# Optimization experiments

Measured on AMD Instinct MI355X. Metric: run time of the kernel, lower is better.

Reference implementation:

```python
import jax, jax.numpy as jnp
import numpy as np

H = 16
EPS = 1e-5

def _layernorm(x, gamma, beta):
    mu = jnp.mean(x, axis=-1, keepdims=True)
    var = jnp.var(x, axis=-1, keepdims=True)
    return (x - mu) * jax.lax.rsqrt(var + EPS) * gamma + beta

def setup_inputs() -> dict:
    key = jax.random.key(0)
    ks = jax.random.split(key, 5)
    B, T, E = 4, 2048, 1024
    D = E // H
    return {
        "x": jax.random.normal(ks[0], (B, T, E), dtype=jnp.float32),
        "Wqkv": jax.random.normal(ks[1], (E, 3 * E), dtype=jnp.float32) * (E ** -0.5),
        "bqkv": jax.random.normal(ks[2], (3 * E,), dtype=jnp.float32) * 0.02,
        "q_gamma": jnp.ones((D,), jnp.float32),
        "q_beta": jnp.zeros((D,), jnp.float32),
        "k_gamma": jnp.ones((D,), jnp.float32),
        "k_beta": jnp.zeros((D,), jnp.float32),
        "Wproj": jax.random.normal(ks[3], (E, E), dtype=jnp.float32) * (E ** -0.5),
        "bproj": jnp.zeros((E,), jnp.float32),
    }

def reference(x, Wqkv, bqkv, q_gamma, q_beta, k_gamma, k_beta, Wproj, bproj):
    B, T, E = x.shape
    D = E // H
    qkv = x @ Wqkv + bqkv                      # [B,T,3E]
    q, k, v = jnp.split(qkv, 3, axis=-1)
    # b t (h d) -> b h t d
    to_heads = lambda a: a.reshape(B, T, H, D).transpose(0, 2, 1, 3)
    q, k, v = to_heads(q), to_heads(k), to_heads(v)
    q = _layernorm(q, q_gamma, q_beta)
    k = _layernorm(k, k_gamma, k_beta)
    scale = 1.0 / jnp.sqrt(jnp.float32(D))
    scores = jnp.einsum('bhtd,bhsd->bhts', q, k) * scale   # [B,H,T,T]
    attn = jax.nn.softmax(scores, axis=-1)
    y = jnp.einsum('bhts,bhsd->bhtd', attn, v)             # [B,H,T,D]
    y = y.transpose(0, 2, 1, 3).reshape(B, T, E)           # b h t d -> b t (h d)
    return y @ Wproj + bproj
```

## Files before the change

### kernel.cpp

```cpp
#include <hip/hip_runtime.h>

#define Hn  16
#define Dh  64
#define Bb  4
#define Tn  2048
#define En  1024
#define Mn  8192
#define N1  3072
#define Kn  1024
#define BHT (Bb*Hn*Tn)

typedef __attribute__((ext_vector_type(8)))  short  short8;
typedef __attribute__((ext_vector_type(4)))  short  short4v;
typedef __attribute__((ext_vector_type(4)))  float  f32x4;
typedef __attribute__((ext_vector_type(8)))  __bf16 bf16x8;

__device__ __forceinline__ float b2f(short s) {
  unsigned u = ((unsigned)(unsigned short)s) << 16;
  return __builtin_bit_cast(float, u);
}
__device__ __forceinline__ short f2b(float f) {
  unsigned u = __builtin_bit_cast(unsigned, f);
  u += 0x7fffu + ((u >> 16) & 1u);
  return (short)(u >> 16);
}
__device__ __forceinline__ f32x4 mfma16(short8 a, short8 b, f32x4 c) {
  return __builtin_amdgcn_mfma_f32_16x16x32_bf16(
      __builtin_bit_cast(bf16x8, a), __builtin_bit_cast(bf16x8, b), c, 0, 0, 0);
}
__device__ __forceinline__ void gload16(const void* g, void* l) {
  __builtin_amdgcn_global_load_lds(
      (const __attribute__((address_space(1))) unsigned int*)g,
      (__attribute__((address_space(3))) unsigned int*)l, 16, 0, 0);
}

__global__ __launch_bounds__(256) void cvt_x_kernel(const float* __restrict__ x,
                                                    short* __restrict__ xb) {
  const size_t i = ((size_t)blockIdx.x * 256 + threadIdx.x) * 8;
  f32x4 a = *(const f32x4*)&x[i];
  f32x4 b = *(const f32x4*)&x[i + 4];
  short8 o;
  o[0]=f2b(a[0]); o[1]=f2b(a[1]); o[2]=f2b(a[2]); o[3]=f2b(a[3]);
  o[4]=f2b(b[0]); o[5]=f2b(b[1]); o[6]=f2b(b[2]); o[7]=f2b(b[3]);
  *(short8*)&xb[i] = o;
}

__global__ __launch_bounds__(256) void transpose_w_kernel(const float* __restrict__ in,
                                                          short* __restrict__ out,
                                                          int R, int C) {
  __shared__ float tile[32][33];
  const int tid = threadIdx.x;
  const int c0 = blockIdx.x * 32, r0 = blockIdx.y * 32;
  const int lr = tid >> 3, lc = (tid & 7) * 4;
  f32x4 v = *(const f32x4*)&in[(size_t)(r0 + lr) * C + c0 + lc];
  tile[lr][lc] = v[0]; tile[lr][lc+1] = v[1]; tile[lr][lc+2] = v[2]; tile[lr][lc+3] = v[3];
  __syncthreads();
  const int oc = tid >> 3, orr = (tid & 7) * 4;
  short4v ov;
  ov[0] = f2b(tile[orr][oc]);   ov[1] = f2b(tile[orr+1][oc]);
  ov[2] = f2b(tile[orr+2][oc]); ov[3] = f2b(tile[orr+3][oc]);
  *(short4v*)&out[(size_t)(c0 + oc) * R + r0 + orr] = ov;
}

template<int MODE>
__global__ __launch_bounds__(256) void gemm_kernel(
    const short* __restrict__ A, const short* __restrict__ Bt,
    const float* __restrict__ bias, float* __restrict__ Cf,
    short* __restrict__ qo, short* __restrict__ ko2, short* __restrict__ vo,
    int N, int NBX, int cpx) {
  __shared__ short As[4096];
  __shared__ short Bs[4096];
  const int lin = blockIdx.x;
  const int swz = (lin & 7) * cpx + (lin >> 3);
  const int bx = swz % NBX, by = swz / NBX;
  const int tid = threadIdx.x, lane = tid & 63, w = tid >> 6;
  const int rowBase = by * 128, colBase = bx * 128;
  f32x4 acc[4][4] = {};
  const int srow = tid >> 2, sk = (tid & 3) << 3;
  const short* Ag = A  + (size_t)(rowBase + srow) * Kn + sk;
  const short* Bg = Bt + (size_t)(colBase + srow) * Kn + sk;
  short* AsW = As + w * 512;
  short* BsW = Bs + w * 512;
  const int ar = (w >> 1) * 64, bc = (w & 1) * 64;
  const int lg8 = (lane >> 4) * 8, lr = lane & 15;

  for (int kt = 0; kt < Kn; kt += 32) {
    __syncthreads();
    gload16(Ag + kt,            AsW);
    gload16(Ag + kt + 64 * Kn,  AsW + 2048);
    gload16(Bg + kt,            BsW);
    gload16(Bg + kt + 64 * Kn,  BsW + 2048);
    __syncthreads();
    short8 af[4], bfr[4];
#pragma unroll
    for (int m = 0; m < 4; ++m) af[m]  = *(const short8*)&As[(ar + m*16 + lr)*32 + lg8];
#pragma unroll
    for (int n = 0; n < 4; ++n) bfr[n] = *(const short8*)&Bs[(bc + n*16 + lr)*32 + lg8];
#pragma unroll
    for (int m = 0; m < 4; ++m)
#pragma unroll
      for (int n = 0; n < 4; ++n)
        acc[m][n] = mfma16(af[m], bfr[n], acc[m][n]);
  }

  const int gr0 = rowBase + ar + (lane >> 4) * 4;
  const int gc0 = colBase + bc + lr;
#pragma unroll
  for (int m = 0; m < 4; ++m) {
#pragma unroll
    for (int n = 0; n < 4; ++n) {
      const int gc = gc0 + n * 16;
      const float bb = bias[gc];
#pragma unroll
      for (int r = 0; r < 4; ++r) {
        const int gr = gr0 + m * 16 + r;
        const float v = acc[m][n][r] + bb;
        if (MODE == 0) {
          Cf[(size_t)gr * N + gc] = v;
        } else {
          const int which = gc >> 10, e = gc & 1023;
          const int hh = e >> 6, d = e & 63;
          const int bidx = gr >> 11, t = gr & 2047;
          const size_t idx = ((size_t)(bidx * Hn + hh) * Tn + t) * Dh + d;
          short* dst = (which == 0) ? qo : (which == 1) ? ko2 : vo;
          dst[idx] = f2b(v);
        }
      }
    }
  }
}

__global__ __launch_bounds__(256) void ln_qk_kernel(short* __restrict__ qp, short* __restrict__ kp,
                                                    const float* __restrict__ qg, const float* __restrict__ qb,
                                                    const float* __restrict__ kg, const float* __restrict__ kb) {
  const int lane = threadIdx.x & 63;
  const int rp = blockIdx.x * 4 + (threadIdx.x >> 6);
  const size_t base = (size_t)rp * 64 + lane;
  float xq = b2f(qp[base]);
  float xk = b2f(kp[base]);
  float sq = xq, sk = xk;
#pragma unroll
  for (int off = 1; off < 64; off <<= 1) { sq += __shfl_xor(sq, off); sk += __shfl_xor(sk, off); }
  const float muq = sq * (1.f/64), muk = sk * (1.f/64);
  const float dq = xq - muq, dk = xk - muk;
  float vq = dq * dq, vk = dk * dk;
#pragma unroll
  for (int off = 1; off < 64; off <<= 1) { vq += __shfl_xor(vq, off); vk += __shfl_xor(vk, off); }
  const float rq = rsqrtf(vq * (1.f/64) + 1e-5f);
  const float rk = rsqrtf(vk * (1.f/64) + 1e-5f);
  const float yq = (dq * rq * qg[lane] + qb[lane]) * (0.125f * 1.44269504088896f);
  const float yk =  dk * rk * kg[lane] + kb[lane];
  qp[base] = f2b(yq);
  kp[base] = f2b(yk);
}

__global__ __launch_bounds__(256) void transpose_v_kernel(const short* __restrict__ vp,
                                                          short* __restrict__ vt) {
  __shared__ short tile[64][72];
  const int tid = threadIdx.x;
  const int bh = blockIdx.y, jt = blockIdx.x;
  const short* src = vp + ((size_t)bh * Tn + jt * 64) * Dh;
#pragma unroll
  for (int i = 0; i < 4; ++i) {
    const int idx = i * 1024 + tid * 4;
    short4v v = *(const short4v*)&src[idx];
    const int r = idx >> 6, c = idx & 63;
    tile[r][c] = v[0]; tile[r][c+1] = v[1]; tile[r][c+2] = v[2]; tile[r][c+3] = v[3];
  }
  __syncthreads();
  short* dst = vt + (size_t)bh * Dh * Tn + jt * 64;
#pragma unroll
  for (int i = 0; i < 4; ++i) {
    const int idx = i * 1024 + tid * 4;
    const int d = idx >> 6, t0 = idx & 63;
    short4v v;
    v[0] = tile[t0][d]; v[1] = tile[t0+1][d]; v[2] = tile[t0+2][d]; v[3] = tile[t0+3][d];
    *(short4v*)&dst[(size_t)d * Tn + t0] = v;
  }
}

__global__ __launch_bounds__(256) void flash_kernel(
    const short* __restrict__ qp, const short* __restrict__ kp,
    const short* __restrict__ vt, short* __restrict__ y) {
  __shared__ short Ks[2][4096];
  __shared__ short Vs[2][4096];
  __shared__ short Ps[8192];
  const int tid = threadIdx.x, lane = tid & 63, w = tid >> 6;
  const int lr = lane & 15, lg = lane >> 4;

  const int j0 = blockIdx.x;
  const int xcd = j0 & 7, kk0 = j0 >> 3;
  const int bh = 8 * xcd + (kk0 & 7), qt = kk0 >> 3;

  const int qrow0 = qt * 128 + w * 32;
  const short* qbase = qp + ((size_t)bh * Tn + qrow0) * Dh;

  short8 aq[2][2];
#pragma unroll
  for (int m = 0; m < 2; ++m)
#pragma unroll
    for (int kk = 0; kk < 2; ++kk)
      aq[m][kk] = *(const short8*)&qbase[(m*16 + lr)*64 + kk*32 + lg*8];

  f32x4 o[2][4] = {};
  float mrow[2][4], lpart[2][4];
#pragma unroll
  for (int m = 0; m < 2; ++m)
#pragma unroll
    for (int r = 0; r < 4; ++r) { mrow[m][r] = -3e38f; lpart[m][r] = 0.f; }

  const int srow = tid >> 3;
  const int sc = (tid & 7) * 8;
  short* Pw = Ps + w * 2048;
  const short* kb = kp + (size_t)bh * Tn * Dh;
  const short* vb = vt + (size_t)bh * Dh * Tn;

#define STAGE(jt, bsel)                                                   \
  {                                                                       \
    _Pragma("unroll")                                                     \
    for (int i = 0; i < 2; ++i) {                                         \
      const int row = i * 32 + srow;                                      \
      const int scs = sc ^ ((row & 7) << 3);                              \
      gload16(kb + (size_t)((jt) * 64 + row) * Dh + scs,                  \
              &Ks[bsel][w * 512 + i * 2048]);                             \
      gload16(vb + (size_t)row * Tn + (jt) * 64 + scs,                    \
              &Vs[bsel][w * 512 + i * 2048]);                             \
    }                                                                     \
  }

  STAGE(0, 0);
  __syncthreads();

  for (int j = 0; j < Tn / 64; ++j) {
    const int cur = j & 1;
    if (j + 1 < Tn / 64) STAGE(j + 1, cur ^ 1);

    short8 bk[4][2];
#pragma unroll
    for (int n = 0; n < 4; ++n)
#pragma unroll
      for (int kk = 0; kk < 2; ++kk) {
        const int row = n * 16 + lr;
        bk[n][kk] = *(const short8*)&Ks[cur][row*64 + ((kk*32 + lg*8) ^ ((row & 7) << 3))];
      }
    f32x4 s[2][4] = {};
    __builtin_amdgcn_s_setprio(1);
#pragma unroll
    for (int m = 0; m < 2; ++m)
#pragma unroll
      for (int n = 0; n < 4; ++n) {
        s[m][n] = mfma16(aq[m][0], bk[n][0], s[m][n]);
        s[m][n] = mfma16(aq[m][1], bk[n][1], s[m][n]);
      }
    __builtin_amdgcn_s_setprio(0);

    float pm[2][4];
#pragma unroll
    for (int m = 0; m < 2; ++m)
#pragma unroll
      for (int r = 0; r < 4; ++r)
        pm[m][r] = fmaxf(fmaxf(s[m][0][r], s[m][1][r]), fmaxf(s[m][2][r], s[m][3][r]));
    int ok = 1;
#pragma unroll
    for (int m = 0; m < 2; ++m)
#pragma unroll
      for (int r = 0; r < 4; ++r)
        ok &= (pm[m][r] <= mrow[m][r] + 11.0f) ? 1 : 0;
    if (!__all(ok)) {
      float tm[2][4];
#pragma unroll
      for (int m = 0; m < 2; ++m)
#pragma unroll
        for (int r = 0; r < 4; ++r) tm[m][r] = pm[m][r];
#pragma unroll
      for (int off = 1; off < 16; off <<= 1)
#pragma unroll
        for (int m = 0; m < 2; ++m)
#pragma unroll
          for (int r = 0; r < 4; ++r)
            tm[m][r] = fmaxf(tm[m][r], __shfl_xor(tm[m][r], off));
#pragma unroll
      for (int m = 0; m < 2; ++m)
#pragma unroll
        for (int r = 0; r < 4; ++r) {
          const float mn = fmaxf(mrow[m][r], tm[m][r]);
          const float corr = __builtin_amdgcn_exp2f(mrow[m][r] - mn);
          lpart[m][r] *= corr;
#pragma unroll
          for (int dn = 0; dn < 4; ++dn) o[m][dn][r] *= corr;
          mrow[m][r] = mn;
        }
    }

#pragma unroll
    for (int m = 0; m < 2; ++m)
#pragma unroll
      for (int n = 0; n < 4; ++n)
#pragma unroll
        for (int r = 0; r < 4; ++r) {
          const float p = __builtin_amdgcn_exp2f(s[m][n][r] - mrow[m][r]);
          const unsigned u = __builtin_bit_cast(unsigned, p);
          lpart[m][r] += __builtin_bit_cast(float, u & 0xffff0000u);
          const int q = m*16 + lg*4 + r;
          const int k = n*16 + lr;
          Pw[q*64 + (k ^ ((q & 7) << 3))] = (short)(u >> 16);
        }

    short8 pa[2][2], bv[4][2];
#pragma unroll
    for (int m = 0; m < 2; ++m)
#pragma unroll
      for (int kk = 0; kk < 2; ++kk) {
        const int q = m*16 + lr;
        pa[m][kk] = *(const short8*)&Pw[q*64 + ((kk*32 + lg*8) ^ ((q & 7) << 3))];
      }
#pragma unroll
    for (int dn = 0; dn < 4; ++dn)
#pragma unroll
      for (int kk = 0; kk < 2; ++kk) {
        const int row = dn * 16 + lr;
        bv[dn][kk] = *(const short8*)&Vs[cur][row*64 + ((kk*32 + lg*8) ^ ((row & 7) << 3))];
      }
    __builtin_amdgcn_s_setprio(1);
#pragma unroll
    for (int m = 0; m < 2; ++m)
#pragma unroll
      for (int dn = 0; dn < 4; ++dn) {
        o[m][dn] = mfma16(pa[m][0], bv[dn][0], o[m][dn]);
        o[m][dn] = mfma16(pa[m][1], bv[dn][1], o[m][dn]);
      }
    __builtin_amdgcn_s_setprio(0);

    __syncthreads();
  }
#undef STAGE

#pragma unroll
  for (int off = 1; off < 16; off <<= 1)
#pragma unroll
    for (int m = 0; m < 2; ++m)
#pragma unroll
      for (int r = 0; r < 4; ++r)
        lpart[m][r] += __shfl_xor(lpart[m][r], off);

  const int b = bh >> 4, hh = bh & 15;
  short* yb = y + (size_t)b * Tn * En + hh * 64;
#pragma unroll
  for (int m = 0; m < 2; ++m)
#pragma unroll
    for (int r = 0; r < 4; ++r) {
      const float rl = 1.0f / lpart[m][r];
      const int t = qrow0 + m*16 + lg*4 + r;
#pragma unroll
      for (int dn = 0; dn < 4; ++dn) {
        const int d = dn*16 + lr;
        yb[(size_t)t * En + d] = f2b(o[m][dn][r] * rl);
      }
    }
}

extern "C" void kernel_launch(void* const* d_in, const int* in_sizes, int n_in,
                              void* d_out, int out_size, void* d_ws, size_t ws_size,
                              hipStream_t stream) {
  const float* x     = (const float*)d_in[0];
  const float* Wqkv  = (const float*)d_in[1];
  const float* bqkv  = (const float*)d_in[2];
  const float* qg    = (const float*)d_in[3];
  const float* qb    = (const float*)d_in[4];
  const float* kg    = (const float*)d_in[5];
  const float* kb    = (const float*)d_in[6];
  const float* Wproj = (const float*)d_in[7];
  const float* bproj = (const float*)d_in[8];
  float* out = (float*)d_out;

  char* p = (char*)d_ws;
  short* xb     = (short*)p; p += (size_t)Mn * Kn * 2;
  short* wqkvT  = (short*)p; p += (size_t)N1 * Kn * 2;
  short* wprojT = (short*)p; p += (size_t)En * Kn * 2;
  short* qp     = (short*)p; p += (size_t)Mn * Kn * 2;
  short* kp     = (short*)p; p += (size_t)Mn * Kn * 2;
  short* vp     = (short*)p; p += (size_t)Mn * Kn * 2;
  short* vtb    = (short*)p; p += (size_t)Mn * Kn * 2;
  short* yb     = (short*)p; p += (size_t)Mn * Kn * 2;

  cvt_x_kernel<<<Mn * Kn / (256 * 8), 256, 0, stream>>>(x, xb);
  transpose_w_kernel<<<dim3(N1 / 32, Kn / 32), 256, 0, stream>>>(Wqkv, wqkvT, Kn, N1);
  transpose_w_kernel<<<dim3(En / 32, Kn / 32), 256, 0, stream>>>(Wproj, wprojT, Kn, En);
  gemm_kernel<1><<<(N1 / 128) * (Mn / 128), 256, 0, stream>>>(
      xb, wqkvT, bqkv, nullptr, qp, kp, vp, N1, N1 / 128, (N1 / 128) * (Mn / 128) / 8);
  ln_qk_kernel<<<BHT / 4, 256, 0, stream>>>(qp, kp, qg, qb, kg, kb);
  transpose_v_kernel<<<dim3(Tn / 64, Bb * Hn), 256, 0, stream>>>(vp, vtb);
  flash_kernel<<<1024, 256, 0, stream>>>(qp, kp, vtb, yb);
  gemm_kernel<0><<<(En / 128) * (Mn / 128), 256, 0, stream>>>(
      yb, wprojT, bproj, out, nullptr, nullptr, nullptr, En, En / 128, (En / 128) * (Mn / 128) / 8);
}
```

Before: 289.9 us.

## Split P·V into two halves and compute row sums via MFMA with ones

The softmax P tile is now written and consumed in two 32-column halves, which halves the per-wave LDS scratch and lets exp/store work on the second half overlap the first half's MFMAs. The row-sum accumulation moves from per-element scalar adds plus a final cross-lane shuffle reduction onto the matrix unit, by multiplying P with a vector of bf16 ones. This removes VALU adds and shuffles but adds two extra MFMAs per half and an extra LDS round trip.

```diff
diff --git a/kernel.cpp b/kernel.cpp
--- a/kernel.cpp
+++ b/kernel.cpp
@@ -184,7 +184,7 @@
     const short* __restrict__ vt, short* __restrict__ y) {
   __shared__ short Ks[2][4096];
   __shared__ short Vs[2][4096];
-  __shared__ short Ps[8192];
+  __shared__ short Ps[4096];
   const int tid = threadIdx.x, lane = tid & 63, w = tid >> 6;
   const int lr = lane & 15, lg = lane >> 4;
 
@@ -202,16 +202,21 @@
     for (int kk = 0; kk < 2; ++kk)
       aq[m][kk] = *(const short8*)&qbase[(m*16 + lr)*64 + kk*32 + lg*8];
 
+  short8 ones;
+#pragma unroll
+  for (int i = 0; i < 8; ++i) ones[i] = (short)0x3F80;
+
   f32x4 o[2][4] = {};
-  float mrow[2][4], lpart[2][4];
+  f32x4 lacc[2] = {};
+  float mrow[2][4];
 #pragma unroll
   for (int m = 0; m < 2; ++m)
 #pragma unroll
-    for (int r = 0; r < 4; ++r) { mrow[m][r] = -3e38f; lpart[m][r] = 0.f; }
+    for (int r = 0; r < 4; ++r) mrow[m][r] = -3e38f;
 
   const int srow = tid >> 3;
   const int sc = (tid & 7) * 8;
-  short* Pw = Ps + w * 2048;
+  short* Pw = Ps + w * 1024;
   const short* kb = kp + (size_t)bh * Tn * Dh;
   const short* vb = vt + (size_t)bh * Dh * Tn;
 
@@ -228,6 +233,8 @@
     }                                                                     \
   }
 
+#define PSW(q) ((((q) & 3) << 3) ^ (((q) & 4) << 2))
+
   STAGE(0, 0);
   __syncthreads();
 
@@ -285,35 +292,14 @@
         for (int r = 0; r < 4; ++r) {
           const float mn = fmaxf(mrow[m][r], tm[m][r]);
           const float corr = __builtin_amdgcn_exp2f(mrow[m][r] - mn);
-          lpart[m][r] *= corr;
+          lacc[m][r] *= corr;
 #pragma unroll
           for (int dn = 0; dn < 4; ++dn) o[m][dn][r] *= corr;
           mrow[m][r] = mn;
         }
     }
 
-#pragma unroll
-    for (int m = 0; m < 2; ++m)
-#pragma unroll
-      for (int n = 0; n < 4; ++n)
-#pragma unroll
-        for (int r = 0; r < 4; ++r) {
-          const float p = __builtin_amdgcn_exp2f(s[m][n][r] - mrow[m][r]);
-          const unsigned u = __builtin_bit_cast(unsigned, p);
-          lpart[m][r] += __builtin_bit_cast(float, u & 0xffff0000u);
-          const int q = m*16 + lg*4 + r;
-          const int k = n*16 + lr;
-          Pw[q*64 + (k ^ ((q & 7) << 3))] = (short)(u >> 16);
-        }
-
-    short8 pa[2][2], bv[4][2];
-#pragma unroll
-    for (int m = 0; m < 2; ++m)
-#pragma unroll
-      for (int kk = 0; kk < 2; ++kk) {
-        const int q = m*16 + lr;
-        pa[m][kk] = *(const short8*)&Pw[q*64 + ((kk*32 + lg*8) ^ ((q & 7) << 3))];
-      }
+    short8 bv[4][2];
 #pragma unroll
     for (int dn = 0; dn < 4; ++dn)
 #pragma unroll
@@ -321,27 +307,65 @@
         const int row = dn * 16 + lr;
         bv[dn][kk] = *(const short8*)&Vs[cur][row*64 + ((kk*32 + lg*8) ^ ((row & 7) << 3))];
       }
+
+#pragma unroll
+    for (int m = 0; m < 2; ++m)
+#pragma unroll
+      for (int n = 0; n < 2; ++n)
+#pragma unroll
+        for (int r = 0; r < 4; ++r) {
+          const float p = __builtin_amdgcn_exp2f(s[m][n][r] - mrow[m][r]);
+          const unsigned u = __builtin_bit_cast(unsigned, p);
+          const int q = m*16 + lg*4 + r;
+          Pw[q*32 + ((n*16 + lr) ^ PSW(q))] = (short)(u >> 16);
+        }
+    short8 pa0[2];
+#pragma unroll
+    for (int m = 0; m < 2; ++m) {
+      const int q = m*16 + lr;
+      pa0[m] = *(const short8*)&Pw[q*32 + ((lg*8) ^ PSW(q))];
+    }
     __builtin_amdgcn_s_setprio(1);
 #pragma unroll
+    for (int m = 0; m < 2; ++m) {
+      lacc[m] = mfma16(pa0[m], ones, lacc[m]);
+#pragma unroll
+      for (int dn = 0; dn < 4; ++dn)
+        o[m][dn] = mfma16(pa0[m], bv[dn][0], o[m][dn]);
+    }
+    __builtin_amdgcn_s_setprio(0);
+
+#pragma unroll
     for (int m = 0; m < 2; ++m)
 #pragma unroll
-      for (int dn = 0; dn < 4; ++dn) {
-        o[m][dn] = mfma16(pa[m][0], bv[dn][0], o[m][dn]);
-        o[m][dn] = mfma16(pa[m][1], bv[dn][1], o[m][dn]);
-      }
+      for (int n = 0; n < 2; ++n)
+#pragma unroll
+        for (int r = 0; r < 4; ++r) {
+          const float p = __builtin_amdgcn_exp2f(s[m][2 + n][r] - mrow[m][r]);
+          const unsigned u = __builtin_bit_cast(unsigned, p);
+          const int q = m*16 + lg*4 + r;
+          Pw[q*32 + ((n*16 + lr) ^ PSW(q))] = (short)(u >> 16);
+        }
+    short8 pa1[2];
+#pragma unroll
+    for (int m = 0; m < 2; ++m) {
+      const int q = m*16 + lr;
+      pa1[m] = *(const short8*)&Pw[q*32 + ((lg*8) ^ PSW(q))];
+    }
+    __builtin_amdgcn_s_setprio(1);
+#pragma unroll
+    for (int m = 0; m < 2; ++m) {
+      lacc[m] = mfma16(pa1[m], ones, lacc[m]);
+#pragma unroll
+      for (int dn = 0; dn < 4; ++dn)
+        o[m][dn] = mfma16(pa1[m], bv[dn][1], o[m][dn]);
+    }
     __builtin_amdgcn_s_setprio(0);
 
     __syncthreads();
   }
 #undef STAGE
-
-#pragma unroll
-  for (int off = 1; off < 16; off <<= 1)
-#pragma unroll
-    for (int m = 0; m < 2; ++m)
-#pragma unroll
-      for (int r = 0; r < 4; ++r)
-        lpart[m][r] += __shfl_xor(lpart[m][r], off);
+#undef PSW
 
   const int b = bh >> 4, hh = bh & 15;
   short* yb = y + (size_t)b * Tn * En + hh * 64;
@@ -349,7 +373,7 @@
   for (int m = 0; m < 2; ++m)
 #pragma unroll
     for (int r = 0; r < 4; ++r) {
-      const float rl = 1.0f / lpart[m][r];
+      const float rl = 1.0f / lacc[m][r];
       const int t = qrow0 + m*16 + lg*4 + r;
 #pragma unroll
       for (int dn = 0; dn < 4; ++dn) {
```

After: 285.9 us. No clear change (-1.4%).
